# Optimization experiments

Measured on AMD Instinct MI355X. Metric: run time of the kernel, lower is better.

The kernel has to match this reference:

```python
import jax, jax.numpy as jnp
import numpy as np

N = 50000    # nodes
E = 600000   # edges
H = 128      # hidden_dim
NF = 12      # n_features
L = 4        # n_layers
EPS = 1e-5   # LayerNorm eps


def setup_inputs() -> dict:
    key = jax.random.key(0)
    ks = jax.random.split(key, 32)

    def w(k, shape, fan_in):
        return (jax.random.normal(k, shape, jnp.float32) / np.float32(np.sqrt(fan_in)))

    inp = {
        "x": jax.random.normal(ks[0], (N, NF), jnp.float32),
        "edge_index": jax.random.randint(ks[1], (2, E), 0, N, dtype=jnp.int64),
        # encoder: Linear(NF,H) -> ReLU -> Linear(H,H)
        "enc_W1": w(ks[2], (NF, H), NF), "enc_b1": jnp.zeros((H,), jnp.float32),
        "enc_W2": w(ks[3], (H, H), H),   "enc_b2": jnp.zeros((H,), jnp.float32),
        # L residual SAGE blocks (PyG SAGEConv: lin_l on mean-aggr w/ bias, lin_r on self no bias)
        "lin_l_W": w(ks[4], (L, H, H), H), "lin_l_b": jnp.zeros((L, H), jnp.float32),
        "lin_r_W": w(ks[5], (L, H, H), H),
        "ln_g": jnp.ones((L, H), jnp.float32), "ln_b": jnp.zeros((L, H), jnp.float32),
        # disp head: H->H->H//2->3
        "dW1": w(ks[6], (H, H), H),      "db1": jnp.zeros((H,), jnp.float32),
        "dW2": w(ks[7], (H, H // 2), H), "db2": jnp.zeros((H // 2,), jnp.float32),
        "dW3": w(ks[8], (H // 2, 3), H // 2), "db3": jnp.zeros((3,), jnp.float32),
        # stress head: H->H->H//2->1
        "sW1": w(ks[9], (H, H), H),       "sb1": jnp.zeros((H,), jnp.float32),
        "sW2": w(ks[10], (H, H // 2), H), "sb2": jnp.zeros((H // 2,), jnp.float32),
        "sW3": w(ks[11], (H // 2, 1), H // 2), "sb3": jnp.zeros((1,), jnp.float32),
    }
    return inp


def reference(x, edge_index, enc_W1, enc_b1, enc_W2, enc_b2,
              lin_l_W, lin_l_b, lin_r_W, ln_g, ln_b,
              dW1, db1, dW2, db2, dW3, db3,
              sW1, sb1, sW2, sb2, sW3, sb3):
    src, dst = edge_index[0], edge_index[1]

    # linear load-scaling ratio from load columns [3:6]
    load_mag = jnp.linalg.norm(x[:, 3:6], axis=1)
    ratio = jnp.max(load_mag)

    # encoder MLP
    h = jnp.maximum(x @ enc_W1 + enc_b1, 0.0) @ enc_W2 + enc_b2  # [N, H]

    # in-degree for mean aggregation (clamped to 1 like PyG)
    deg = jax.ops.segment_sum(jnp.ones((E,), h.dtype), dst, num_segments=N)
    inv_deg = 1.0 / jnp.clip(deg, 1.0)[:, None]  # [N, 1]

    for l in range(L):
        # SAGEConv: mean of neighbor (src) features at dst, then lin_l(aggr) + lin_r(self)
        agg = jax.ops.segment_sum(h[src], dst, num_segments=N) * inv_deg  # [N, H]
        y = agg @ lin_l_W[l] + lin_l_b[l] + h @ lin_r_W[l]
        # LayerNorm over channels
        mu = jnp.mean(y, axis=-1, keepdims=True)
        var = jnp.var(y, axis=-1, keepdims=True)
        y = (y - mu) * jax.lax.rsqrt(var + EPS) * ln_g[l] + ln_b[l]
        # residual + ReLU
        h = h + jnp.maximum(y, 0.0)

    # heads
    d = jnp.maximum(h @ dW1 + db1, 0.0)
    d = jnp.maximum(d @ dW2 + db2, 0.0) @ dW3 + db3  # [N, 3]
    s = jnp.maximum(h @ sW1 + sb1, 0.0)
    s = jnp.maximum(s @ sW2 + sb2, 0.0) @ sW3 + sb3  # [N, 1]

    # linear_scaling = True
    d = d * ratio
    s = s * ratio
    return jnp.concatenate([d, s], axis=1)  # [N, 4]
```

## Files before the change

### kernel.cpp

```cpp
#include <hip/hip_runtime.h>
#include <hip/hip_bf16.h>

typedef __hip_bfloat16 bf16;
typedef short bf16x8 __attribute__((ext_vector_type(8)));
typedef float f32x4 __attribute__((ext_vector_type(4)));

__device__ __forceinline__ float2 bfpair(unsigned u){
  float2 r; r.x = __uint_as_float(u<<16); r.y = __uint_as_float(u & 0xffff0000u); return r;
}
__device__ __forceinline__ float bfu(unsigned short u){ return __uint_as_float(((unsigned)u)<<16); }
__device__ __forceinline__ unsigned f2bf(float f){
  unsigned u = __float_as_uint(f);
  return (u + 0x7fffu + ((u>>16)&1u)) >> 16;
}
__device__ __forceinline__ unsigned fpack(float a, float b){
  return (f2bf(b)<<16) | f2bf(a);
}
__device__ __forceinline__ int edge_is64(const int* e){
  return (e[1]==0) & (e[3]==0) & (e[5]==0);
}
__device__ __forceinline__ int edge_ld(const int* e, int is64, int idx){
  return e[is64 ? 2*idx : idx];
}

__global__ void k_pre(const float* __restrict__ x, const int* __restrict__ eidx,
                      unsigned* __restrict__ ratio, int* __restrict__ deg,
                      int N, int E, int nbE){
  if((int)blockIdx.x < nbE){
    int e = blockIdx.x*blockDim.x + threadIdx.x;
    if(e>=E) return;
    int is64 = edge_is64(eidx);
    int d = edge_ld(eidx, is64, E+e);
    if((unsigned)d < (unsigned)N) atomicAdd(&deg[d], 1);
  } else {
    int i = (blockIdx.x-nbE)*blockDim.x + threadIdx.x;
    int stride = 256*blockDim.x;
    float m = 0.f;
    for(; i<N; i+=stride){
      float a = x[(size_t)i*12+3];
      float b = x[(size_t)i*12+4];
      float c = x[(size_t)i*12+5];
      m = fmaxf(m, sqrtf(a*a+b*b+c*c));
    }
    #pragma unroll
    for(int off=1; off<64; off<<=1) m = fmaxf(m, __shfl_xor(m, off));
    if((threadIdx.x & 63)==0) atomicMax(ratio, __float_as_uint(m));
  }
}

__global__ void k_scan1(const int* __restrict__ deg, int* __restrict__ bsum, int N){
  int t = threadIdx.x;
  int idx0 = blockIdx.x*1024 + t*4;
  int s=0;
  #pragma unroll
  for(int i=0;i<4;i++){ int idx=idx0+i; if(idx<N) s += deg[idx]; }
  #pragma unroll
  for(int off=1; off<64; off<<=1) s += __shfl_xor(s, off);
  __shared__ int ws4[4];
  if((t&63)==0) ws4[t>>6]=s;
  __syncthreads();
  if(t==0) bsum[blockIdx.x]=ws4[0]+ws4[1]+ws4[2]+ws4[3];
}
__global__ void k_scan3(const int* __restrict__ deg, const int* __restrict__ bsum,
                        int* __restrict__ offs, int* __restrict__ pos,
                        float* __restrict__ invdeg, int N, int E, int nb){
  __shared__ int sb[64];
  int t = threadIdx.x;
  if(t < 64){
    int v = (t<nb)? bsum[t] : 0;
    int incl = v;
    #pragma unroll
    for(int off=1; off<64; off<<=1){ int u = __shfl_up(incl, (unsigned)off); if(t>=off) incl+=u; }
    sb[t] = incl - v;
  }
  __syncthreads();
  int idx0 = blockIdx.x*1024 + t*4;
  int d[4]; int s=0;
  #pragma unroll
  for(int i=0;i<4;i++){ int idx=idx0+i; d[i] = (idx<N)? deg[idx]:0; s+=d[i]; }
  int lane=t&63, w=t>>6;
  int incl=s;
  #pragma unroll
  for(int off=1; off<64; off<<=1){ int v=__shfl_up(incl, (unsigned)off); if(lane>=off) incl+=v; }
  __shared__ int wsum[4];
  if(lane==63) wsum[w]=incl;
  __syncthreads();
  int base = sb[blockIdx.x];
  for(int i=0;i<w;i++) base += wsum[i];
  int run = base + incl - s;
  #pragma unroll
  for(int i=0;i<4;i++){
    int idx=idx0+i;
    if(idx<N){
      offs[idx]=run; pos[idx]=run;
      invdeg[idx] = 1.0f / (float)(d[i]>0? d[i]:1);
    }
    run += d[i];
  }
  if(blockIdx.x==0 && t==0) offs[N]=E;
}

__global__ void k_bucket_wconv(
    const int* __restrict__ eidx, int* __restrict__ pos, int* __restrict__ csr,
    int E, int N, int nbE,
    const float* __restrict__ llW, const float* __restrict__ lrW,
    const float* __restrict__ dW1, const float* __restrict__ sW1,
    const float* __restrict__ dW2, const float* __restrict__ sW2,
    const float* __restrict__ eW2,
    unsigned short* __restrict__ WTs, unsigned short* __restrict__ WT1,
    unsigned short* __restrict__ WT2, unsigned short* __restrict__ WE2){
  if((int)blockIdx.x < nbE){
    int e = blockIdx.x*256 + threadIdx.x;
    if(e>=E) return;
    int is64 = edge_is64(eidx);
    int d = edge_ld(eidx, is64, E+e);
    int s = edge_ld(eidx, is64, e);
    if((unsigned)d >= (unsigned)N) return;
    if((unsigned)s >= (unsigned)N) s = 0;
    int p = atomicAdd(&pos[d], 1);
    if((unsigned)p < (unsigned)E) csr[p] = s;
    return;
  }
  int idx = (blockIdx.x - nbE)*256 + threadIdx.x;
  int j = idx & 7;
  int lane = (idx>>3) & 63;
  int q = lane >> 4, p = lane & 15;
  if(idx < 131072){
    int nt = (idx>>9) & 7, ks = (idx>>12) & 7, l = (idx>>15) & 3;
    int k = ks*32 + q*8 + j, n = nt*16 + p;
    float v = (k<128) ? llW[(size_t)l*16384 + (size_t)k*128 + n]
                      : lrW[(size_t)l*16384 + (size_t)(k-128)*128 + n];
    WTs[idx] = (unsigned short)f2bf(v);
  } else if(idx < 163840){
    int i2 = idx - 131072;
    int nt = (i2>>9) & 15, ks = (i2>>13) & 3;
    int k = ks*32 + q*8 + j, n = nt*16 + p;
    float v = (n<128) ? dW1[(size_t)k*128 + n] : sW1[(size_t)k*128 + (n-128)];
    WT1[i2] = (unsigned short)f2bf(v);
  } else if(idx < 180224){
    int i2 = idx - 163840;
    int nt = (i2>>9) & 7, ks = (i2>>12) & 3;
    int k = ks*32 + q*8 + j, n = nt*16 + p;
    float v = (n<64) ? dW2[(size_t)k*64 + n] : sW2[(size_t)k*64 + (n-64)];
    WT2[i2] = (unsigned short)f2bf(v);
  } else if(idx < 196608){
    int i2 = idx - 180224;
    int nt = (i2>>9) & 7, ks = (i2>>12) & 3;
    int k = ks*32 + q*8 + j, n = nt*16 + p;
    WE2[i2] = (unsigned short)f2bf(eW2[(size_t)k*128 + n]);
  }
}

__global__ __launch_bounds__(256) void k_aggregate(
    const bf16* __restrict__ h, bf16* __restrict__ agg,
    const int* __restrict__ offs, const int* __restrict__ csr,
    const float* __restrict__ invdeg, int N, int E){
  int row = blockIdx.x*16 + (threadIdx.x>>4);
  int l = threadIdx.x & 15;
  if(row >= N) return;
  int s = offs[row], e = offs[row+1];
  s = max(0, min(s, E)); e = max(s, min(e, E));
  float a0=0.f,a1=0.f,a2=0.f,a3=0.f,a4=0.f,a5=0.f,a6=0.f,a7=0.f;
  int i = s;
  for(; i+4<=e; i+=4){
    int j0=csr[i], j1=csr[i+1], j2=csr[i+2], j3=csr[i+3];
    uint4 u0 = *(const uint4*)(h + (size_t)j0*128 + l*8);
    uint4 u1 = *(const uint4*)(h + (size_t)j1*128 + l*8);
    uint4 u2 = *(const uint4*)(h + (size_t)j2*128 + l*8);
    uint4 u3 = *(const uint4*)(h + (size_t)j3*128 + l*8);
    float2 f;
    f=bfpair(u0.x); a0+=f.x; a1+=f.y;  f=bfpair(u0.y); a2+=f.x; a3+=f.y;
    f=bfpair(u0.z); a4+=f.x; a5+=f.y;  f=bfpair(u0.w); a6+=f.x; a7+=f.y;
    f=bfpair(u1.x); a0+=f.x; a1+=f.y;  f=bfpair(u1.y); a2+=f.x; a3+=f.y;
    f=bfpair(u1.z); a4+=f.x; a5+=f.y;  f=bfpair(u1.w); a6+=f.x; a7+=f.y;
    f=bfpair(u2.x); a0+=f.x; a1+=f.y;  f=bfpair(u2.y); a2+=f.x; a3+=f.y;
    f=bfpair(u2.z); a4+=f.x; a5+=f.y;  f=bfpair(u2.w); a6+=f.x; a7+=f.y;
    f=bfpair(u3.x); a0+=f.x; a1+=f.y;  f=bfpair(u3.y); a2+=f.x; a3+=f.y;
    f=bfpair(u3.z); a4+=f.x; a5+=f.y;  f=bfpair(u3.w); a6+=f.x; a7+=f.y;
  }
  for(; i<e; ++i){
    int jj = csr[i];
    uint4 u = *(const uint4*)(h + (size_t)jj*128 + l*8);
    float2 f;
    f=bfpair(u.x); a0+=f.x; a1+=f.y;  f=bfpair(u.y); a2+=f.x; a3+=f.y;
    f=bfpair(u.z); a4+=f.x; a5+=f.y;  f=bfpair(u.w); a6+=f.x; a7+=f.y;
  }
  float id = invdeg[row];
  uint4 o;
  o.x = fpack(a0*id, a1*id); o.y = fpack(a2*id, a3*id);
  o.z = fpack(a4*id, a5*id); o.w = fpack(a6*id, a7*id);
  *(uint4*)(agg + (size_t)row*128 + l*8) = o;
}

__global__ __launch_bounds__(256) void k_encoder(
  const float* __restrict__ x,
  const float* __restrict__ W1, const float* __restrict__ b1,
  const unsigned short* __restrict__ WE2, const float* __restrict__ b2,
  bf16* __restrict__ h, int N)
{
  __shared__ float Xs[64][12];
  __shared__ float W1s[12][128];
  __shared__ float b1s[128];
  __shared__ __align__(16) unsigned short T1b[64][136];
  int tid = threadIdx.x;
  int tx = tid & 31, ty = tid >> 5;
  int rowBase = blockIdx.x*64;
  for(int idx=tid; idx<768; idx+=256){
    int r = idx/12, c = idx - r*12;
    int row = rowBase + r;
    Xs[r][c] = (row<N)? x[(size_t)row*12+c] : 0.f;
  }
  for(int idx=tid; idx<1536; idx+=256) W1s[idx>>7][idx&127] = W1[idx];
  if(tid<128) b1s[tid] = b1[tid];
  __syncthreads();
  float acc[8][4] = {};
  #pragma unroll
  for(int k=0;k<12;k++){
    float4 w4 = *(float4*)&W1s[k][tx*4];
    #pragma unroll
    for(int r=0;r<8;r++){
      float a = Xs[ty*8+r][k];
      acc[r][0]+=a*w4.x; acc[r][1]+=a*w4.y; acc[r][2]+=a*w4.z; acc[r][3]+=a*w4.w;
    }
  }
  #pragma unroll
  for(int r=0;r<8;r++)
    #pragma unroll
    for(int c=0;c<4;c++)
      T1b[ty*8+r][tx*4+c] = (unsigned short)f2bf(fmaxf(acc[r][c] + b1s[tx*4+c], 0.f));
  __syncthreads();

  int lane = tid & 63;
  int w = tid >> 6, q = lane >> 4, p = lane & 15;
  f32x4 acc2[8];
  #pragma unroll
  for(int nt=0; nt<8; nt++) acc2[nt] = (f32x4){0.f,0.f,0.f,0.f};
  #pragma unroll
  for(int ks=0; ks<4; ks++){
    bf16x8 af = *(const bf16x8*)&T1b[w*16+p][ks*32+q*8];
    #pragma unroll
    for(int nt=0; nt<8; nt++){
      bf16x8 bfr = *(const bf16x8*)(WE2 + ((size_t)(ks*8+nt)*64 + lane)*8);
      acc2[nt] = __builtin_amdgcn_mfma_f32_16x16x32_bf16(af, bfr, acc2[nt], 0,0,0);
    }
  }
  float b2v[8];
  #pragma unroll
  for(int nt=0; nt<8; nt++) b2v[nt] = b2[nt*16+p];
  unsigned short* hu = (unsigned short*)h;
  #pragma unroll
  for(int r=0;r<4;r++){
    int row = rowBase + w*16 + q*4 + r;
    if(row < N){
      #pragma unroll
      for(int nt=0; nt<8; nt++)
        hu[(size_t)row*128 + nt*16+p] = (unsigned short)f2bf(acc2[nt][r] + b2v[nt]);
    }
  }
}

__global__ __launch_bounds__(256) void k_sage_mfma(
    bf16* __restrict__ h, const bf16* __restrict__ agg,
    const unsigned short* __restrict__ WT,
    const float* __restrict__ bl, const float* __restrict__ lng,
    const float* __restrict__ lnb, int N)
{
  int tid = threadIdx.x;
  int lane = tid & 63;
  int w = tid >> 6;
  int q = lane >> 4;
  int p = lane & 15;
  int rowBase = blockIdx.x*64;

  int am = rowBase + w*16 + p;
  bool arow_ok = am < N;
  const unsigned short* aggRow = (const unsigned short*)agg + (size_t)am*128;
  const unsigned short* hRow   = (const unsigned short*)h   + (size_t)am*128;

  f32x4 acc[8];
  #pragma unroll
  for(int nt=0; nt<8; nt++) acc[nt] = (f32x4){0.f,0.f,0.f,0.f};

  #pragma unroll
  for(int ks=0; ks<8; ks++){
    int koff = ks*32 + q*8;
    bf16x8 afrag = {0,0,0,0,0,0,0,0};
    if(arow_ok){
      const unsigned short* src = (koff < 128) ? (aggRow + koff) : (hRow + (koff-128));
      afrag = *(const bf16x8*)src;
    }
    #pragma unroll
    for(int nt=0; nt<8; nt++){
      bf16x8 bfrag = *(const bf16x8*)(WT + ((size_t)(ks*8+nt)*64 + lane)*8);
      acc[nt] = __builtin_amdgcn_mfma_f32_16x16x32_bf16(afrag, bfrag, acc[nt], 0, 0, 0);
    }
  }

  float blv[8], gvv[8], bvv[8];
  #pragma unroll
  for(int nt=0; nt<8; nt++){
    int col = nt*16 + p;
    blv[nt] = bl[col]; gvv[nt] = lng[col]; bvv[nt] = lnb[col];
  }
  unsigned short* hu = (unsigned short*)h;
  #pragma unroll
  for(int r=0; r<4; r++){
    int row = rowBase + w*16 + q*4 + r;
    float y[8]; float s = 0.f, sq = 0.f;
    #pragma unroll
    for(int nt=0; nt<8; nt++){
      float v = acc[nt][r] + blv[nt];
      y[nt] = v; s += v; sq += v*v;
    }
    #pragma unroll
    for(int off=1; off<16; off<<=1){ s += __shfl_xor(s, off); sq += __shfl_xor(sq, off); }
    float mu = s*(1.f/128.f);
    float var = fmaxf(sq*(1.f/128.f) - mu*mu, 0.f);
    float rstd = rsqrtf(var + 1e-5f);
    if(row < N){
      #pragma unroll
      for(int nt=0; nt<8; nt++){
        int col = nt*16 + p;
        float hv = bfu(hu[(size_t)row*128 + col]);
        float o = hv + fmaxf((y[nt]-mu)*rstd*gvv[nt] + bvv[nt], 0.f);
        hu[(size_t)row*128 + col] = (unsigned short)f2bf(o);
      }
    }
  }
}

__global__ __launch_bounds__(256) void k_heads_mfma(
  const bf16* __restrict__ h,
  const unsigned short* __restrict__ WT1,
  const unsigned short* __restrict__ WT2,
  const float* __restrict__ db1, const float* __restrict__ sb1,
  const float* __restrict__ db2, const float* __restrict__ sb2,
  const float* __restrict__ dW3, const float* __restrict__ db3,
  const float* __restrict__ sW3, const float* __restrict__ sb3,
  const float* __restrict__ ratio_p, float* __restrict__ out, int N)
{
  __shared__ __align__(16) unsigned short T1s[4][16][264];
  const float ratio = *ratio_p;
  int tid = threadIdx.x;
  int lane = tid & 63;
  int w = tid >> 6;
  int q = lane >> 4;
  int p = lane & 15;
  int rowBase = blockIdx.x*64;
  int am = rowBase + w*16 + p;
  bool arow_ok = am < N;
  const unsigned short* hRow = (const unsigned short*)h + (size_t)am*128;

  f32x4 acc1[16];
  #pragma unroll
  for(int nt=0; nt<16; nt++) acc1[nt] = (f32x4){0.f,0.f,0.f,0.f};
  #pragma unroll
  for(int ks=0; ks<4; ks++){
    int koff = ks*32 + q*8;
    bf16x8 af = {0,0,0,0,0,0,0,0};
    if(arow_ok) af = *(const bf16x8*)(hRow + koff);
    #pragma unroll
    for(int nt=0; nt<16; nt++){
      bf16x8 bfr = *(const bf16x8*)(WT1 + ((size_t)(ks*16+nt)*64 + lane)*8);
      acc1[nt] = __builtin_amdgcn_mfma_f32_16x16x32_bf16(af, bfr, acc1[nt], 0,0,0);
    }
  }
  #pragma unroll
  for(int nt=0; nt<16; nt++){
    float b1v = (nt<8) ? db1[nt*16+p] : sb1[(nt-8)*16+p];
    #pragma unroll
    for(int r=0;r<4;r++){
      float v = fmaxf(acc1[nt][r] + b1v, 0.f);
      T1s[w][q*4+r][nt*16+p] = (unsigned short)f2bf(v);
    }
  }
  __syncthreads();

  f32x4 acc2[8];
  #pragma unroll
  for(int nt=0; nt<8; nt++) acc2[nt] = (f32x4){0.f,0.f,0.f,0.f};
  #pragma unroll
  for(int ks=0; ks<4; ks++){
    int koff = ks*32 + q*8;
    bf16x8 ad = *(const bf16x8*)&T1s[w][p][koff];
    bf16x8 as = *(const bf16x8*)&T1s[w][p][128+koff];
    #pragma unroll
    for(int nt=0; nt<8; nt++){
      bf16x8 bfr = *(const bf16x8*)(WT2 + ((size_t)(ks*8+nt)*64 + lane)*8);
      acc2[nt] = __builtin_amdgcn_mfma_f32_16x16x32_bf16(nt<4? ad : as, bfr, acc2[nt], 0,0,0);
    }
  }

  float w3d[4][3], w3s[4], bd2[4], bs2[4];
  #pragma unroll
  for(int nt=0; nt<4; nt++){
    #pragma unroll
    for(int c=0;c<3;c++) w3d[nt][c] = dW3[(nt*16+p)*3 + c];
    w3s[nt] = sW3[nt*16+p];
    bd2[nt] = db2[nt*16+p];
    bs2[nt] = sb2[nt*16+p];
  }
  float b3v = (p==0)? db3[0] : (p==1)? db3[1] : (p==2)? db3[2] : sb3[0];
  #pragma unroll
  for(int r=0;r<4;r++){
    int row = rowBase + w*16 + q*4 + r;
    float pd0=0.f, pd1=0.f, pd2=0.f, ps=0.f;
    #pragma unroll
    for(int nt=0; nt<4; nt++){
      float td = fmaxf(acc2[nt][r]   + bd2[nt], 0.f);
      float ts = fmaxf(acc2[nt+4][r] + bs2[nt], 0.f);
      pd0 += td*w3d[nt][0]; pd1 += td*w3d[nt][1]; pd2 += td*w3d[nt][2];
      ps  += ts*w3s[nt];
    }
    #pragma unroll
    for(int off=1; off<16; off<<=1){
      pd0 += __shfl_xor(pd0, off); pd1 += __shfl_xor(pd1, off);
      pd2 += __shfl_xor(pd2, off); ps  += __shfl_xor(ps, off);
    }
    if(row < N && p < 4){
      float v = (p==0)? pd0 : (p==1)? pd1 : (p==2)? pd2 : ps;
      out[(size_t)row*4 + p] = (v + b3v)*ratio;
    }
  }
}

extern "C" void kernel_launch(void* const* d_in, const int* in_sizes, int n_in,
                              void* d_out, int out_size, void* d_ws, size_t ws_size,
                              hipStream_t stream)
{
  const float* x   = (const float*)d_in[0];
  const int*  eidx = (const int*) d_in[1];
  const float* eW1 = (const float*)d_in[2];
  const float* eb1 = (const float*)d_in[3];
  const float* eW2 = (const float*)d_in[4];
  const float* eb2 = (const float*)d_in[5];
  const float* llW = (const float*)d_in[6];
  const float* llb = (const float*)d_in[7];
  const float* lrW = (const float*)d_in[8];
  const float* lng = (const float*)d_in[9];
  const float* lnb = (const float*)d_in[10];
  const float* dW1 = (const float*)d_in[11];
  const float* db1 = (const float*)d_in[12];
  const float* dW2 = (const float*)d_in[13];
  const float* db2 = (const float*)d_in[14];
  const float* dW3 = (const float*)d_in[15];
  const float* db3 = (const float*)d_in[16];
  const float* sW1 = (const float*)d_in[17];
  const float* sb1 = (const float*)d_in[18];
  const float* sW2 = (const float*)d_in[19];
  const float* sb2 = (const float*)d_in[20];
  const float* sW3 = (const float*)d_in[21];
  const float* sb3 = (const float*)d_in[22];
  float* out = (float*)d_out;

  const int N = in_sizes[0] / 12;
  const int E = in_sizes[1] / 2;
  (void)n_in; (void)out_size; (void)ws_size;

  char* base = (char*)d_ws;
  size_t off = 0;
  auto alloc = [&](size_t nbytes)->char*{
    char* p = base + off; off += (nbytes + 255) & ~(size_t)255; return p;
  };
  unsigned* ratio = (unsigned*)alloc(4);
  int*   deg    = (int*)  alloc((size_t)N*4);
  int*   offs   = (int*)  alloc(((size_t)N+1)*4);
  int*   pos    = (int*)  alloc((size_t)N*4);
  int*   bsum   = (int*)  alloc(256*4);
  int*   csr    = (int*)  alloc((size_t)E*4);
  float* invdeg = (float*)alloc((size_t)N*4);
  bf16*  hA     = (bf16*) alloc((size_t)N*128*2);
  bf16*  agg    = (bf16*) alloc((size_t)N*128*2);
  unsigned short* WTs  = (unsigned short*)alloc((size_t)131072*2);
  unsigned short* WT1h = (unsigned short*)alloc((size_t)32768*2);
  unsigned short* WT2h = (unsigned short*)alloc((size_t)16384*2);
  unsigned short* WE2  = (unsigned short*)alloc((size_t)16384*2);

  size_t zbytes = (size_t)((char*)offs - base);
  hipMemsetAsync(d_ws, 0, zbytes, stream);

  int nbE    = (E + 255)/256;
  int nbScan = (N + 1023)/1024;
  int nbTile = (N + 63)/64;
  int nbAgg  = (N + 15)/16;

  k_pre  <<<nbE + 256, 256, 0, stream>>>(x, eidx, ratio, deg, N, E, nbE);
  k_scan1<<<nbScan, 256, 0, stream>>>(deg, bsum, N);
  k_scan3<<<nbScan, 256, 0, stream>>>(deg, bsum, offs, pos, invdeg, N, E, nbScan);
  k_bucket_wconv<<<nbE + 768, 256, 0, stream>>>(eidx, pos, csr, E, N, nbE,
      llW, lrW, dW1, sW1, dW2, sW2, eW2, WTs, WT1h, WT2h, WE2);

  k_encoder<<<nbTile, 256, 0, stream>>>(x, eW1, eb1, WE2, eb2, hA, N);
  for(int l=0;l<4;l++){
    k_aggregate<<<nbAgg, 256, 0, stream>>>(hA, agg, offs, csr, invdeg, N, E);
    k_sage_mfma<<<nbTile, 256, 0, stream>>>(hA, agg,
        WTs + (size_t)l*32768,
        llb + (size_t)l*128, lng + (size_t)l*128, lnb + (size_t)l*128, N);
  }
  k_heads_mfma<<<nbTile, 256, 0, stream>>>(hA, WT1h, WT2h,
      db1, sb1, db2, sb2, dW3, db3, sW3, sb3, (const float*)ratio, out, N);
}
```

Before: 376.6 us.

## Fuse neighbor aggregation into SAGE MFMA layer kernel with ping-pong buffers

Merges the per-layer gather/mean aggregation and the MFMA linear+LayerNorm+residual into one kernel with 16-row tiles. The aggregated rows stay in shared memory instead of going through a global agg buffer, and the layer reads h from one buffer and writes to another. Each wave now computes two of the eight column tiles, and LayerNorm statistics are reduced across waves through shared memory. Weight conversion also moves from the bucket kernel into the pre kernel. The cost is smaller MFMA tiles, so each block reloads weights for only 16 rows, and an extra block barrier.

```diff
diff --git a/kernel.cpp b/kernel.cpp
--- a/kernel.cpp
+++ b/kernel.cpp
@@ -25,103 +25,38 @@
 
 __global__ void k_pre(const float* __restrict__ x, const int* __restrict__ eidx,
                       unsigned* __restrict__ ratio, int* __restrict__ deg,
-                      int N, int E, int nbE){
-  if((int)blockIdx.x < nbE){
-    int e = blockIdx.x*blockDim.x + threadIdx.x;
+                      int N, int E, int nbE,
+                      const float* __restrict__ llW, const float* __restrict__ lrW,
+                      const float* __restrict__ dW1, const float* __restrict__ sW1,
+                      const float* __restrict__ dW2, const float* __restrict__ sW2,
+                      const float* __restrict__ eW2,
+                      unsigned short* __restrict__ WTs, unsigned short* __restrict__ WT1,
+                      unsigned short* __restrict__ WT2, unsigned short* __restrict__ WE2){
+  int b = (int)blockIdx.x;
+  if(b < nbE){
+    int e = b*256 + threadIdx.x;
     if(e>=E) return;
     int is64 = edge_is64(eidx);
     int d = edge_ld(eidx, is64, E+e);
     if((unsigned)d < (unsigned)N) atomicAdd(&deg[d], 1);
-  } else {
-    int i = (blockIdx.x-nbE)*blockDim.x + threadIdx.x;
-    int stride = 256*blockDim.x;
+    return;
+  }
+  if(b < nbE + 256){
+    int i = (b-nbE)*256 + threadIdx.x;
+    int stride = 256*256;
     float m = 0.f;
     for(; i<N; i+=stride){
       float a = x[(size_t)i*12+3];
-      float b = x[(size_t)i*12+4];
+      float bb = x[(size_t)i*12+4];
       float c = x[(size_t)i*12+5];
-      m = fmaxf(m, sqrtf(a*a+b*b+c*c));
+      m = fmaxf(m, sqrtf(a*a+bb*bb+c*c));
     }
     #pragma unroll
     for(int off=1; off<64; off<<=1) m = fmaxf(m, __shfl_xor(m, off));
     if((threadIdx.x & 63)==0) atomicMax(ratio, __float_as_uint(m));
-  }
-}
-
-__global__ void k_scan1(const int* __restrict__ deg, int* __restrict__ bsum, int N){
-  int t = threadIdx.x;
-  int idx0 = blockIdx.x*1024 + t*4;
-  int s=0;
-  #pragma unroll
-  for(int i=0;i<4;i++){ int idx=idx0+i; if(idx<N) s += deg[idx]; }
-  #pragma unroll
-  for(int off=1; off<64; off<<=1) s += __shfl_xor(s, off);
-  __shared__ int ws4[4];
-  if((t&63)==0) ws4[t>>6]=s;
-  __syncthreads();
-  if(t==0) bsum[blockIdx.x]=ws4[0]+ws4[1]+ws4[2]+ws4[3];
-}
-__global__ void k_scan3(const int* __restrict__ deg, const int* __restrict__ bsum,
-                        int* __restrict__ offs, int* __restrict__ pos,
-                        float* __restrict__ invdeg, int N, int E, int nb){
-  __shared__ int sb[64];
-  int t = threadIdx.x;
-  if(t < 64){
-    int v = (t<nb)? bsum[t] : 0;
-    int incl = v;
-    #pragma unroll
-    for(int off=1; off<64; off<<=1){ int u = __shfl_up(incl, (unsigned)off); if(t>=off) incl+=u; }
-    sb[t] = incl - v;
-  }
-  __syncthreads();
-  int idx0 = blockIdx.x*1024 + t*4;
-  int d[4]; int s=0;
-  #pragma unroll
-  for(int i=0;i<4;i++){ int idx=idx0+i; d[i] = (idx<N)? deg[idx]:0; s+=d[i]; }
-  int lane=t&63, w=t>>6;
-  int incl=s;
-  #pragma unroll
-  for(int off=1; off<64; off<<=1){ int v=__shfl_up(incl, (unsigned)off); if(lane>=off) incl+=v; }
-  __shared__ int wsum[4];
-  if(lane==63) wsum[w]=incl;
-  __syncthreads();
-  int base = sb[blockIdx.x];
-  for(int i=0;i<w;i++) base += wsum[i];
-  int run = base + incl - s;
-  #pragma unroll
-  for(int i=0;i<4;i++){
-    int idx=idx0+i;
-    if(idx<N){
-      offs[idx]=run; pos[idx]=run;
-      invdeg[idx] = 1.0f / (float)(d[i]>0? d[i]:1);
-    }
-    run += d[i];
-  }
-  if(blockIdx.x==0 && t==0) offs[N]=E;
-}
-
-__global__ void k_bucket_wconv(
-    const int* __restrict__ eidx, int* __restrict__ pos, int* __restrict__ csr,
-    int E, int N, int nbE,
-    const float* __restrict__ llW, const float* __restrict__ lrW,
-    const float* __restrict__ dW1, const float* __restrict__ sW1,
-    const float* __restrict__ dW2, const float* __restrict__ sW2,
-    const float* __restrict__ eW2,
-    unsigned short* __restrict__ WTs, unsigned short* __restrict__ WT1,
-    unsigned short* __restrict__ WT2, unsigned short* __restrict__ WE2){
-  if((int)blockIdx.x < nbE){
-    int e = blockIdx.x*256 + threadIdx.x;
-    if(e>=E) return;
-    int is64 = edge_is64(eidx);
-    int d = edge_ld(eidx, is64, E+e);
-    int s = edge_ld(eidx, is64, e);
-    if((unsigned)d >= (unsigned)N) return;
-    if((unsigned)s >= (unsigned)N) s = 0;
-    int p = atomicAdd(&pos[d], 1);
-    if((unsigned)p < (unsigned)E) csr[p] = s;
     return;
   }
-  int idx = (blockIdx.x - nbE)*256 + threadIdx.x;
+  int idx = (b - nbE - 256)*256 + threadIdx.x;
   int j = idx & 7;
   int lane = (idx>>3) & 63;
   int q = lane >> 4, p = lane & 15;
@@ -151,45 +86,69 @@
   }
 }
 
-__global__ __launch_bounds__(256) void k_aggregate(
-    const bf16* __restrict__ h, bf16* __restrict__ agg,
-    const int* __restrict__ offs, const int* __restrict__ csr,
-    const float* __restrict__ invdeg, int N, int E){
-  int row = blockIdx.x*16 + (threadIdx.x>>4);
-  int l = threadIdx.x & 15;
-  if(row >= N) return;
-  int s = offs[row], e = offs[row+1];
-  s = max(0, min(s, E)); e = max(s, min(e, E));
-  float a0=0.f,a1=0.f,a2=0.f,a3=0.f,a4=0.f,a5=0.f,a6=0.f,a7=0.f;
-  int i = s;
-  for(; i+4<=e; i+=4){
-    int j0=csr[i], j1=csr[i+1], j2=csr[i+2], j3=csr[i+3];
-    uint4 u0 = *(const uint4*)(h + (size_t)j0*128 + l*8);
-    uint4 u1 = *(const uint4*)(h + (size_t)j1*128 + l*8);
-    uint4 u2 = *(const uint4*)(h + (size_t)j2*128 + l*8);
-    uint4 u3 = *(const uint4*)(h + (size_t)j3*128 + l*8);
-    float2 f;
-    f=bfpair(u0.x); a0+=f.x; a1+=f.y;  f=bfpair(u0.y); a2+=f.x; a3+=f.y;
-    f=bfpair(u0.z); a4+=f.x; a5+=f.y;  f=bfpair(u0.w); a6+=f.x; a7+=f.y;
-    f=bfpair(u1.x); a0+=f.x; a1+=f.y;  f=bfpair(u1.y); a2+=f.x; a3+=f.y;
-    f=bfpair(u1.z); a4+=f.x; a5+=f.y;  f=bfpair(u1.w); a6+=f.x; a7+=f.y;
-    f=bfpair(u2.x); a0+=f.x; a1+=f.y;  f=bfpair(u2.y); a2+=f.x; a3+=f.y;
-    f=bfpair(u2.z); a4+=f.x; a5+=f.y;  f=bfpair(u2.w); a6+=f.x; a7+=f.y;
-    f=bfpair(u3.x); a0+=f.x; a1+=f.y;  f=bfpair(u3.y); a2+=f.x; a3+=f.y;
-    f=bfpair(u3.z); a4+=f.x; a5+=f.y;  f=bfpair(u3.w); a6+=f.x; a7+=f.y;
-  }
-  for(; i<e; ++i){
-    int jj = csr[i];
-    uint4 u = *(const uint4*)(h + (size_t)jj*128 + l*8);
-    float2 f;
-    f=bfpair(u.x); a0+=f.x; a1+=f.y;  f=bfpair(u.y); a2+=f.x; a3+=f.y;
-    f=bfpair(u.z); a4+=f.x; a5+=f.y;  f=bfpair(u.w); a6+=f.x; a7+=f.y;
-  }
-  float id = invdeg[row];
-  uint4 o;
-  o.x = fpack(a0*id, a1*id); o.y = fpack(a2*id, a3*id);
-  o.z = fpack(a4*id, a5*id); o.w = fpack(a6*id, a7*id);
-  *(uint4*)(agg + (size_t)row*128 + l*8) = o;
+__global__ void k_scan1(const int* __restrict__ deg, int* __restrict__ bsum, int N){
+  int t = threadIdx.x;
+  int idx0 = blockIdx.x*1024 + t*4;
+  int s=0;
+  #pragma unroll
+  for(int i=0;i<4;i++){ int idx=idx0+i; if(idx<N) s += deg[idx]; }
+  #pragma unroll
+  for(int off=1; off<64; off<<=1) s += __shfl_xor(s, off);
+  __shared__ int ws4[4];
+  if((t&63)==0) ws4[t>>6]=s;
+  __syncthreads();
+  if(t==0) bsum[blockIdx.x]=ws4[0]+ws4[1]+ws4[2]+ws4[3];
+}
+__global__ void k_scan3(const int* __restrict__ deg, const int* __restrict__ bsum,
+                        int* __restrict__ offs, int* __restrict__ pos,
+                        float* __restrict__ invdeg, int N, int E, int nb){
+  __shared__ int sb[64];
+  int t = threadIdx.x;
+  if(t < 64){
+    int v = (t<nb)? bsum[t] : 0;
+    int incl = v;
+    #pragma unroll
+    for(int off=1; off<64; off<<=1){ int u = __shfl_up(incl, (unsigned)off); if(t>=off) incl+=u; }
+    sb[t] = incl - v;
+  }
+  __syncthreads();
+  int idx0 = blockIdx.x*1024 + t*4;
+  int d[4]; int s=0;
+  #pragma unroll
+  for(int i=0;i<4;i++){ int idx=idx0+i; d[i] = (idx<N)? deg[idx]:0; s+=d[i]; }
+  int lane=t&63, w=t>>6;
+  int incl=s;
+  #pragma unroll
+  for(int off=1; off<64; off<<=1){ int v=__shfl_up(incl, (unsigned)off); if(lane>=off) incl+=v; }
+  __shared__ int wsum[4];
+  if(lane==63) wsum[w]=incl;
+  __syncthreads();
+  int base = sb[blockIdx.x];
+  for(int i=0;i<w;i++) base += wsum[i];
+  int run = base + incl - s;
+  #pragma unroll
+  for(int i=0;i<4;i++){
+    int idx=idx0+i;
+    if(idx<N){
+      offs[idx]=run; pos[idx]=run;
+      invdeg[idx] = 1.0f / (float)(d[i]>0? d[i]:1);
+    }
+    run += d[i];
+  }
+  if(blockIdx.x==0 && t==0) offs[N]=E;
+}
+
+__global__ void k_bucket(const int* __restrict__ eidx, int* __restrict__ pos,
+                         int* __restrict__ csr, int E, int N){
+  int e = blockIdx.x*blockDim.x + threadIdx.x;
+  if(e>=E) return;
+  int is64 = edge_is64(eidx);
+  int d = edge_ld(eidx, is64, E+e);
+  int s = edge_ld(eidx, is64, e);
+  if((unsigned)d >= (unsigned)N) return;
+  if((unsigned)s >= (unsigned)N) s = 0;
+  int p = atomicAdd(&pos[d], 1);
+  if((unsigned)p < (unsigned)E) csr[p] = s;
 }
 
 __global__ __launch_bounds__(256) void k_encoder(
@@ -259,72 +218,122 @@
   }
 }
 
-__global__ __launch_bounds__(256) void k_sage_mfma(
-    bf16* __restrict__ h, const bf16* __restrict__ agg,
+__global__ __launch_bounds__(256) void k_layer16(
+    const bf16* __restrict__ hin, bf16* __restrict__ hout,
+    const int* __restrict__ offs, const int* __restrict__ csr,
+    const float* __restrict__ invdeg,
     const unsigned short* __restrict__ WT,
     const float* __restrict__ bl, const float* __restrict__ lng,
-    const float* __restrict__ lnb, int N)
+    const float* __restrict__ lnb, int N, int E)
 {
+  __shared__ __align__(16) unsigned short Ag[16][136];
+  __shared__ float sPart[4][16];
+  __shared__ float qPart[4][16];
   int tid = threadIdx.x;
+  int rowBase = blockIdx.x*16;
+
+  {
+    int qw = tid >> 4;
+    int l  = tid & 15;
+    int row = rowBase + qw;
+    float a0=0.f,a1=0.f,a2=0.f,a3=0.f,a4=0.f,a5=0.f,a6=0.f,a7=0.f;
+    if(row < N){
+      int s = offs[row], e = offs[row+1];
+      s = max(0, min(s, E)); e = max(s, min(e, E));
+      int i = s;
+      for(; i+4<=e; i+=4){
+        int j0=csr[i], j1=csr[i+1], j2=csr[i+2], j3=csr[i+3];
+        uint4 u0 = *(const uint4*)(hin + (size_t)j0*128 + l*8);
+        uint4 u1 = *(const uint4*)(hin + (size_t)j1*128 + l*8);
+        uint4 u2 = *(const uint4*)(hin + (size_t)j2*128 + l*8);
+        uint4 u3 = *(const uint4*)(hin + (size_t)j3*128 + l*8);
+        float2 f;
+        f=bfpair(u0.x); a0+=f.x; a1+=f.y;  f=bfpair(u0.y); a2+=f.x; a3+=f.y;
+        f=bfpair(u0.z); a4+=f.x; a5+=f.y;  f=bfpair(u0.w); a6+=f.x; a7+=f.y;
+        f=bfpair(u1.x); a0+=f.x; a1+=f.y;  f=bfpair(u1.y); a2+=f.x; a3+=f.y;
+        f=bfpair(u1.z); a4+=f.x; a5+=f.y;  f=bfpair(u1.w); a6+=f.x; a7+=f.y;
+        f=bfpair(u2.x); a0+=f.x; a1+=f.y;  f=bfpair(u2.y); a2+=f.x; a3+=f.y;
+        f=bfpair(u2.z); a4+=f.x; a5+=f.y;  f=bfpair(u2.w); a6+=f.x; a7+=f.y;
+        f=bfpair(u3.x); a0+=f.x; a1+=f.y;  f=bfpair(u3.y); a2+=f.x; a3+=f.y;
+        f=bfpair(u3.z); a4+=f.x; a5+=f.y;  f=bfpair(u3.w); a6+=f.x; a7+=f.y;
+      }
+      for(; i<e; ++i){
+        int jj = csr[i];
+        uint4 u = *(const uint4*)(hin + (size_t)jj*128 + l*8);
+        float2 f;
+        f=bfpair(u.x); a0+=f.x; a1+=f.y;  f=bfpair(u.y); a2+=f.x; a3+=f.y;
+        f=bfpair(u.z); a4+=f.x; a5+=f.y;  f=bfpair(u.w); a6+=f.x; a7+=f.y;
+      }
+      float id = invdeg[row];
+      a0*=id; a1*=id; a2*=id; a3*=id; a4*=id; a5*=id; a6*=id; a7*=id;
+    }
+    uint4 o;
+    o.x = fpack(a0,a1); o.y = fpack(a2,a3);
+    o.z = fpack(a4,a5); o.w = fpack(a6,a7);
+    *(uint4*)&Ag[qw][l*8] = o;
+  }
+  __syncthreads();
+
   int lane = tid & 63;
   int w = tid >> 6;
   int q = lane >> 4;
   int p = lane & 15;
-  int rowBase = blockIdx.x*64;
-
-  int am = rowBase + w*16 + p;
-  bool arow_ok = am < N;
-  const unsigned short* aggRow = (const unsigned short*)agg + (size_t)am*128;
-  const unsigned short* hRow   = (const unsigned short*)h   + (size_t)am*128;
-
-  f32x4 acc[8];
-  #pragma unroll
-  for(int nt=0; nt<8; nt++) acc[nt] = (f32x4){0.f,0.f,0.f,0.f};
-
+  int nt0 = 2*w, nt1 = 2*w+1;
+  int am = rowBase + p;
+  bool ok = am < N;
+  const unsigned short* hRow = (const unsigned short*)hin + (size_t)am*128;
+
+  f32x4 accA = (f32x4){0.f,0.f,0.f,0.f};
+  f32x4 accB = (f32x4){0.f,0.f,0.f,0.f};
   #pragma unroll
   for(int ks=0; ks<8; ks++){
-    int koff = ks*32 + q*8;
-    bf16x8 afrag = {0,0,0,0,0,0,0,0};
-    if(arow_ok){
-      const unsigned short* src = (koff < 128) ? (aggRow + koff) : (hRow + (koff-128));
-      afrag = *(const bf16x8*)src;
-    }
-    #pragma unroll
-    for(int nt=0; nt<8; nt++){
-      bf16x8 bfrag = *(const bf16x8*)(WT + ((size_t)(ks*8+nt)*64 + lane)*8);
-      acc[nt] = __builtin_amdgcn_mfma_f32_16x16x32_bf16(afrag, bfrag, acc[nt], 0, 0, 0);
-    }
-  }
-
-  float blv[8], gvv[8], bvv[8];
-  #pragma unroll
-  for(int nt=0; nt<8; nt++){
-    int col = nt*16 + p;
-    blv[nt] = bl[col]; gvv[nt] = lng[col]; bvv[nt] = lnb[col];
-  }
-  unsigned short* hu = (unsigned short*)h;
-  #pragma unroll
-  for(int r=0; r<4; r++){
-    int row = rowBase + w*16 + q*4 + r;
-    float y[8]; float s = 0.f, sq = 0.f;
-    #pragma unroll
-    for(int nt=0; nt<8; nt++){
-      float v = acc[nt][r] + blv[nt];
-      y[nt] = v; s += v; sq += v*v;
-    }
+    bf16x8 af;
+    if(ks < 4){
+      af = *(const bf16x8*)&Ag[p][ks*32 + q*8];
+    } else {
+      af = (bf16x8){0,0,0,0,0,0,0,0};
+      if(ok) af = *(const bf16x8*)(hRow + (ks-4)*32 + q*8);
+    }
+    bf16x8 b0 = *(const bf16x8*)(WT + ((size_t)(ks*8+nt0)*64 + lane)*8);
+    bf16x8 b1 = *(const bf16x8*)(WT + ((size_t)(ks*8+nt1)*64 + lane)*8);
+    accA = __builtin_amdgcn_mfma_f32_16x16x32_bf16(af, b0, accA, 0,0,0);
+    accB = __builtin_amdgcn_mfma_f32_16x16x32_bf16(af, b1, accB, 0,0,0);
+  }
+
+  int c0 = nt0*16 + p, c1 = nt1*16 + p;
+  float bl0 = bl[c0], g0 = lng[c0], lb0 = lnb[c0];
+  float bl1 = bl[c1], g1 = lng[c1], lb1 = lnb[c1];
+  float y0[4], y1[4];
+  #pragma unroll
+  for(int r=0;r<4;r++){
+    y0[r] = accA[r] + bl0;
+    y1[r] = accB[r] + bl1;
+    float s  = y0[r] + y1[r];
+    float sq = y0[r]*y0[r] + y1[r]*y1[r];
     #pragma unroll
     for(int off=1; off<16; off<<=1){ s += __shfl_xor(s, off); sq += __shfl_xor(sq, off); }
+    if(p==0){ sPart[w][q*4+r] = s; qPart[w][q*4+r] = sq; }
+  }
+  __syncthreads();
+
+  const unsigned short* hiu = (const unsigned short*)hin;
+  unsigned short* hou = (unsigned short*)hout;
+  #pragma unroll
+  for(int r=0;r<4;r++){
+    int rloc = q*4 + r;
+    float s  = sPart[0][rloc]+sPart[1][rloc]+sPart[2][rloc]+sPart[3][rloc];
+    float sq = qPart[0][rloc]+qPart[1][rloc]+qPart[2][rloc]+qPart[3][rloc];
     float mu = s*(1.f/128.f);
     float var = fmaxf(sq*(1.f/128.f) - mu*mu, 0.f);
     float rstd = rsqrtf(var + 1e-5f);
+    int row = rowBase + rloc;
     if(row < N){
-      #pragma unroll
-      for(int nt=0; nt<8; nt++){
-        int col = nt*16 + p;
-        float hv = bfu(hu[(size_t)row*128 + col]);
-        float o = hv + fmaxf((y[nt]-mu)*rstd*gvv[nt] + bvv[nt], 0.f);
-        hu[(size_t)row*128 + col] = (unsigned short)f2bf(o);
-      }
+      float h0 = bfu(hiu[(size_t)row*128 + c0]);
+      float h1 = bfu(hiu[(size_t)row*128 + c1]);
+      float o0 = h0 + fmaxf((y0[r]-mu)*rstd*g0 + lb0, 0.f);
+      float o1 = h1 + fmaxf((y1[r]-mu)*rstd*g1 + lb1, 0.f);
+      hou[(size_t)row*128 + c0] = (unsigned short)f2bf(o0);
+      hou[(size_t)row*128 + c1] = (unsigned short)f2bf(o1);
     }
   }
 }
@@ -470,7 +479,7 @@
   int*   csr    = (int*)  alloc((size_t)E*4);
   float* invdeg = (float*)alloc((size_t)N*4);
   bf16*  hA     = (bf16*) alloc((size_t)N*128*2);
-  bf16*  agg    = (bf16*) alloc((size_t)N*128*2);
+  bf16*  hB     = (bf16*) alloc((size_t)N*128*2);
   unsigned short* WTs  = (unsigned short*)alloc((size_t)131072*2);
   unsigned short* WT1h = (unsigned short*)alloc((size_t)32768*2);
   unsigned short* WT2h = (unsigned short*)alloc((size_t)16384*2);
@@ -482,21 +491,22 @@
   int nbE    = (E + 255)/256;
   int nbScan = (N + 1023)/1024;
   int nbTile = (N + 63)/64;
-  int nbAgg  = (N + 15)/16;
-
-  k_pre  <<<nbE + 256, 256, 0, stream>>>(x, eidx, ratio, deg, N, E, nbE);
+  int nbLay  = (N + 15)/16;
+
+  k_pre  <<<nbE + 256 + 768, 256, 0, stream>>>(x, eidx, ratio, deg, N, E, nbE,
+      llW, lrW, dW1, sW1, dW2, sW2, eW2, WTs, WT1h, WT2h, WE2);
   k_scan1<<<nbScan, 256, 0, stream>>>(deg, bsum, N);
   k_scan3<<<nbScan, 256, 0, stream>>>(deg, bsum, offs, pos, invdeg, N, E, nbScan);
-  k_bucket_wconv<<<nbE + 768, 256, 0, stream>>>(eidx, pos, csr, E, N, nbE,
-      llW, lrW, dW1, sW1, dW2, sW2, eW2, WTs, WT1h, WT2h, WE2);
+  k_bucket<<<nbE, 256, 0, stream>>>(eidx, pos, csr, E, N);
 
   k_encoder<<<nbTile, 256, 0, stream>>>(x, eW1, eb1, WE2, eb2, hA, N);
+  bf16* hin = hA; bf16* hout = hB;
   for(int l=0;l<4;l++){
-    k_aggregate<<<nbAgg, 256, 0, stream>>>(hA, agg, offs, csr, invdeg, N, E);
-    k_sage_mfma<<<nbTile, 256, 0, stream>>>(hA, agg,
+    k_layer16<<<nbLay, 256, 0, stream>>>(hin, hout, offs, csr, invdeg,
         WTs + (size_t)l*32768,
-        llb + (size_t)l*128, lng + (size_t)l*128, lnb + (size_t)l*128, N);
-  }
-  k_heads_mfma<<<nbTile, 256, 0, stream>>>(hA, WT1h, WT2h,
+        llb + (size_t)l*128, lng + (size_t)l*128, lnb + (size_t)l*128, N, E);
+    bf16* t = hin; hin = hout; hout = t;
+  }
+  k_heads_mfma<<<nbTile, 256, 0, stream>>>(hin, WT1h, WT2h,
       db1, sb1, db2, sb2, dW3, db3, sW3, sb3, (const float*)ratio, out, N);
 }
```

After: 353.4 us. 1.07x faster.
